# Performance work log

Measured on AMD Instinct MI355X. Metric: run time of the kernel, lower is better.

The kernel has to match this reference:

```python
import jax, jax.numpy as jnp
import numpy as np


def _conv(x, w):
    # stride-2, pad-1, 3x3 conv, NCHW activations, HWIO kernel
    return jax.lax.conv_general_dilated(
        x, w, (2, 2), [(1, 1), (1, 1)],
        dimension_numbers=('NCHW', 'HWIO', 'NCHW'))


def setup_inputs() -> dict:
    key = jax.random.key(0)
    ks = iter(jax.random.split(key, 40))
    def rn(shape, scale=1.0):
        return jax.random.normal(next(ks), shape, jnp.float32) * scale
    d = {}
    d['img'] = rn((64, 3, 128, 128))
    d['qst'] = rn((64, 128))
    d['conv_w0'] = rn((3, 3, 3, 24), 1.0 / np.sqrt(3 * 9))
    for i in (1, 2, 3):
        d['conv_w%d' % i] = rn((3, 3, 24, 24), 1.0 / np.sqrt(24 * 9))
    for i in range(4):
        d['bn_s%d' % i] = jax.random.uniform(next(ks), (24,), jnp.float32, 0.5, 1.5)
        d['bn_b%d' % i] = rn((24,), 0.1)
    d['g_w1'] = rn((180, 256), 1.0 / np.sqrt(180))
    d['g_b1'] = rn((256,), 0.01)
    for i in (2, 3, 4):
        d['g_w%d' % i] = rn((256, 256), 1.0 / np.sqrt(256))
        d['g_b%d' % i] = rn((256,), 0.01)
    d['f_w1'] = rn((256, 256), 1.0 / np.sqrt(256))
    d['f_b1'] = rn((256,), 0.01)
    d['f_w2'] = rn((256, 256), 1.0 / np.sqrt(256))
    d['f_b2'] = rn((256,), 0.01)
    d['cls_w'] = rn((256, 32), 1.0 / np.sqrt(256))
    d['cls_b'] = rn((32,), 0.01)
    return d


def reference(img, qst, conv_w0, conv_w1, conv_w2, conv_w3,
              bn_s0, bn_b0, bn_s1, bn_b1, bn_s2, bn_b2, bn_s3, bn_b3,
              g_w1, g_b1, g_w2, g_b2, g_w3, g_b3, g_w4, g_b4,
              f_w1, f_b1, f_w2, f_b2, cls_w, cls_b):
    x = img
    for w, s, b in ((conv_w0, bn_s0, bn_b0), (conv_w1, bn_s1, bn_b1),
                    (conv_w2, bn_s2, bn_b2), (conv_w3, bn_s3, bn_b3)):
        x = jax.nn.relu(_conv(x, w) * s[None, :, None, None] + b[None, :, None, None])
    N, C, H, W = x.shape  # [64, 24, 8, 8]
    # positional encoding: coords_x, coords_y in [-1,1]
    cx, cy = jnp.meshgrid(jnp.linspace(-1.0, 1.0, W), jnp.linspace(-1.0, 1.0, H))
    pos = jnp.broadcast_to(jnp.stack([cx, cy])[None], (N, 2, H, W)).astype(x.dtype)
    x = jnp.concatenate([x, pos], axis=1)              # [N, C+2, H, W]
    Cf = C + 2
    x = x.transpose(0, 2, 3, 1).reshape(N, H * W, Cf)  # [N, HW, 26]
    # RN_G first linear decomposed over concat([x_i, x_j, qst]) so the huge
    # [N, HW, HW, 2C+q] concat tensor is never materialized (same math).
    W1a, W1b, W1c = g_w1[:Cf], g_w1[Cf:2 * Cf], g_w1[2 * Cf:]
    hi = x @ W1a                      # [N, HW, 256]
    hj = x @ W1b                      # [N, HW, 256]
    hq = qst @ W1c + g_b1             # [N, 256]
    h = jax.nn.relu(hi[:, :, None, :] + hj[:, None, :, :] + hq[:, None, None, :])  # [N,HW,HW,256]
    h = jax.nn.relu(h @ g_w2 + g_b2)
    h = jax.nn.relu(h @ g_w3 + g_b3)
    h = jax.nn.relu(h @ g_w4 + g_b4)
    s = h.sum(axis=(1, 2))            # sum over all HW*HW pairs -> [N, 256]
    # RN_F (dropout is identity in eval mode)
    y = jax.nn.relu(s @ f_w1 + f_b1)
    y = jax.nn.relu(y @ f_w2 + f_b2)
    return jax.nn.log_softmax(y @ cls_w + cls_b, axis=1)
```

## Files before the change

### kernel.cpp

```cpp
#include <hip/hip_runtime.h>
#include <hip/hip_bf16.h>
#include <math.h>

typedef __bf16 bf16x8 __attribute__((ext_vector_type(8)));
typedef __bf16 bf16x4 __attribute__((ext_vector_type(4)));
typedef float  f32x4  __attribute__((ext_vector_type(4)));

#define LH 264

__global__ __launch_bounds__(256) void conv0_k(const float* __restrict__ x, const float* __restrict__ w,
                                               const float* __restrict__ sc, const float* __restrict__ bi,
                                               float* __restrict__ y) {
  const int H = 128, W = 128, OH = 64, OW = 64;
  __shared__ float wl[9 * 3 * 24];
  for (int i = threadIdx.x; i < 9 * 3 * 24; i += 256) wl[i] = w[i];
  __syncthreads();

  int idx = blockIdx.x * 256 + threadIdx.x;
  int oxh = idx & 31; int t = idx >> 5; int oy = t & 63; int n = t >> 6;
  int ox0 = oxh * 2;

  float acc0[24], acc1[24];
#pragma unroll
  for (int co = 0; co < 24; ++co) { acc0[co] = 0.f; acc1[co] = 0.f; }

  for (int ci = 0; ci < 3; ++ci) {
    const float* xp = x + (size_t)(n * 3 + ci) * H * W;
#pragma unroll
    for (int ky = 0; ky < 3; ++ky) {
      int iy = 2 * oy + ky - 1;
      if (iy < 0 || iy >= H) continue;
      const float* row = xp + (size_t)iy * W;
      int ixb = 2 * ox0 - 1;
      float in[7];
#pragma unroll
      for (int u = 0; u < 7; ++u) {
        int ix = ixb + u;
        in[u] = (ix >= 0 && ix < W) ? row[ix] : 0.f;
      }
#pragma unroll
      for (int kx = 0; kx < 3; ++kx) {
        const float* wp = &wl[((ky * 3 + kx) * 3 + ci) * 24];
        float v0 = in[kx], v1 = in[kx + 2];
#pragma unroll
        for (int co = 0; co < 24; ++co) {
          float wv = wp[co];
          acc0[co] += v0 * wv;
          acc1[co] += v1 * wv;
        }
      }
    }
  }
  float* yp = y + (size_t)n * 24 * OH * OW + (size_t)oy * OW + ox0;
#pragma unroll
  for (int co = 0; co < 24; ++co) {
    float s = sc[co], b = bi[co];
    yp[(size_t)co * OH * OW]     = fmaxf(acc0[co] * s + b, 0.f);
    yp[(size_t)co * OH * OW + 1] = fmaxf(acc1[co] * s + b, 0.f);
  }
}

__global__ __launch_bounds__(256) void conv1_k(const float* __restrict__ x, const float* __restrict__ w,
                                               const float* __restrict__ sc, const float* __restrict__ bi,
                                               float* __restrict__ y) {
  const int H = 64, W = 64, OH = 32, OW = 32;
  __shared__ float wl[9 * 24 * 12];
  const int half = blockIdx.x & 1, sb = blockIdx.x >> 1;
  for (int i = threadIdx.x; i < 2592; i += 256) {
    int co = i % 12, rest = i / 12;
    wl[i] = w[rest * 24 + half * 12 + co];
  }
  __syncthreads();

  int idx = sb * 256 + threadIdx.x;
  int oxh = idx & 15; int tt = idx >> 4; int oy = tt & 31; int n = tt >> 5;
  int ox0 = oxh * 2;

  float acc0[12], acc1[12];
#pragma unroll
  for (int co = 0; co < 12; ++co) { acc0[co] = 0.f; acc1[co] = 0.f; }

  for (int ci = 0; ci < 24; ++ci) {
    const float* xp = x + (size_t)(n * 24 + ci) * H * W;
#pragma unroll
    for (int ky = 0; ky < 3; ++ky) {
      int iy = 2 * oy + ky - 1;
      if (iy < 0 || iy >= H) continue;
      const float* row = xp + (size_t)iy * W;
      int ixb = 2 * ox0 - 1;
      float in[7];
#pragma unroll
      for (int u = 0; u < 7; ++u) {
        int ix = ixb + u;
        in[u] = (ix >= 0 && ix < W) ? row[ix] : 0.f;
      }
#pragma unroll
      for (int kx = 0; kx < 3; ++kx) {
        const float* wp = &wl[((ky * 3 + kx) * 24 + ci) * 12];
        float v0 = in[kx], v1 = in[kx + 2];
#pragma unroll
        for (int co = 0; co < 12; ++co) {
          float wv = wp[co];
          acc0[co] += v0 * wv;
          acc1[co] += v1 * wv;
        }
      }
    }
  }
  float* yp = y + (size_t)n * 24 * OH * OW + (size_t)(half * 12) * OH * OW + (size_t)oy * OW + ox0;
#pragma unroll
  for (int co = 0; co < 12; ++co) {
    int cog = half * 12 + co;
    float s = sc[cog], b = bi[cog];
    yp[(size_t)co * OH * OW]     = fmaxf(acc0[co] * s + b, 0.f);
    yp[(size_t)co * OH * OW + 1] = fmaxf(acc1[co] * s + b, 0.f);
  }
}

__global__ __launch_bounds__(256) void mid_k(const float* __restrict__ c1,
    const float* __restrict__ w2, const float* __restrict__ bs2, const float* __restrict__ bb2,
    const float* __restrict__ gw1, const float* __restrict__ gb1, const float* __restrict__ qst,
    const float* __restrict__ g2, const float* __restrict__ g3, const float* __restrict__ g4,
    float* __restrict__ c2, float* __restrict__ hq, __bf16* __restrict__ Wt,
    float* __restrict__ sbuf) {
  __shared__ float smem[8224];
  const int blk = blockIdx.x, t = threadIdx.x;

  if (blk < 128) {
    const int half = blk & 1, sb = blk >> 1;
    for (int i = t; i < 2592; i += 256) {
      int co = i % 12, rest = i / 12;
      smem[i] = w2[rest * 24 + half * 12 + co];
    }
    __syncthreads();
    int idx = sb * 256 + t;
    int ox = idx & 15, oy = (idx >> 4) & 15, n = idx >> 8;
    const int H = 32, W = 32, OH = 16, OW = 16;
    float acc[12];
#pragma unroll
    for (int co = 0; co < 12; ++co) acc[co] = 0.f;
    for (int ci = 0; ci < 24; ++ci) {
      const float* xp = c1 + (size_t)(n * 24 + ci) * H * W;
#pragma unroll
      for (int ky = 0; ky < 3; ++ky) {
        int iy = 2 * oy + ky - 1;
        if (iy < 0 || iy >= H) continue;
#pragma unroll
        for (int kx = 0; kx < 3; ++kx) {
          int ix = 2 * ox + kx - 1;
          if (ix < 0 || ix >= W) continue;
          float v = xp[(size_t)iy * W + ix];
          const float* wp = &smem[((ky * 3 + kx) * 24 + ci) * 12];
#pragma unroll
          for (int co = 0; co < 12; ++co) acc[co] += v * wp[co];
        }
      }
    }
    float* yp = c2 + (size_t)n * 24 * OH * OW + (size_t)(half * 12) * OH * OW + (size_t)oy * OW + ox;
#pragma unroll
    for (int co = 0; co < 12; ++co) {
      int cog = half * 12 + co;
      yp[(size_t)co * OH * OW] = fmaxf(acc[co] * bs2[cog] + bb2[cog], 0.f);
    }

  } else if (blk < 152) {
    float* tile = smem;
    const int lb = blk - 128;
    const int l = lb >> 3, ks = lb & 7;
    const float* src = (l == 0) ? g2 : (l == 1) ? g3 : g4;
    for (int kk = 0; kk < 32; ++kk) tile[kk * 257 + t] = src[(ks * 32 + kk) * 256 + t];
    __syncthreads();
    const int q = t & 3, nb = t >> 2;
    __bf16* out = Wt + (size_t)(l * 8 + ks) * 8192;
#pragma unroll
    for (int i = 0; i < 4; ++i) {
      int nn = i * 64 + nb;
      bf16x8 v;
#pragma unroll
      for (int j = 0; j < 8; ++j) v[j] = (__bf16)tile[(q * 8 + j) * 257 + nn];
      *(bf16x8*)&out[nn * 32 + q * 8] = v;
    }

  } else {
    const int n = blk - 152;
    sbuf[n * 256 + t] = 0.f;
    float* qs = smem;
    if (t < 128) qs[t] = qst[n * 128 + t];
    __syncthreads();
    float a = gb1[t];
    for (int c = 0; c < 128; ++c) a += qs[c] * gw1[(52 + c) * 256 + t];
    hq[n * 256 + t] = a;
  }
}

__global__ __launch_bounds__(256) void tail_k(const float* __restrict__ c2,
    const float* __restrict__ w3, const float* __restrict__ bs3, const float* __restrict__ bb3,
    const float* __restrict__ gw1, float* __restrict__ hi, float* __restrict__ hj) {
  __shared__ float w3l[5184];
  __shared__ float cs2[6144];
  __shared__ float s3[1536];
  const int n = blockIdx.x, t = threadIdx.x;
  for (int i = t; i < 5184; i += 256) w3l[i] = w3[i];
  for (int i = t; i < 6144; i += 256) cs2[i] = c2[(size_t)n * 6144 + i];
  __syncthreads();

  const int pos = t & 63, cog = t >> 6;
  const int oy = pos >> 3, ox = pos & 7;
  float acc[6];
#pragma unroll
  for (int u = 0; u < 6; ++u) acc[u] = 0.f;
  for (int ci = 0; ci < 24; ++ci) {
    const float* cp = &cs2[ci * 256];
#pragma unroll
    for (int ky = 0; ky < 3; ++ky) {
      int iy = 2 * oy + ky - 1;
      if (iy < 0 || iy >= 16) continue;
#pragma unroll
      for (int kx = 0; kx < 3; ++kx) {
        int ix = 2 * ox + kx - 1;
        if (ix < 0 || ix >= 16) continue;
        float v = cp[iy * 16 + ix];
        const float* wp = &w3l[((ky * 3 + kx) * 24 + ci) * 24 + cog * 6];
#pragma unroll
        for (int u = 0; u < 6; ++u) acc[u] += v * wp[u];
      }
    }
  }
#pragma unroll
  for (int u = 0; u < 6; ++u) {
    int co = cog * 6 + u;
    s3[co * 64 + pos] = fmaxf(acc[u] * bs3[co] + bb3[co], 0.f);
  }

  float wa[26], wb[26];
#pragma unroll
  for (int c = 0; c < 26; ++c) {
    wa[c] = gw1[c * 256 + t];
    wb[c] = gw1[(26 + c) * 256 + t];
  }
  __syncthreads();
  for (int p = 0; p < 64; ++p) {
    float a = 0.f, b = 0.f;
#pragma unroll
    for (int c = 0; c < 24; ++c) {
      float v = s3[c * 64 + p];
      a += v * wa[c];
      b += v * wb[c];
    }
    float cx = -1.f + (2.f / 7.f) * (float)(p & 7);
    float cy = -1.f + (2.f / 7.f) * (float)(p >> 3);
    a += cx * wa[24] + cy * wa[25];
    b += cx * wb[24] + cy * wb[25];
    hi[(size_t)(n * 64 + p) * 256 + t] = a;
    hj[(size_t)(n * 64 + p) * 256 + t] = b;
  }
}

__global__ __launch_bounds__(256, 2)
void g_fused(const float* __restrict__ hi, const float* __restrict__ hj,
             const float* __restrict__ hq, const __bf16* __restrict__ Wt,
             const float* __restrict__ b2, const float* __restrict__ b3,
             const float* __restrict__ b4, float* __restrict__ s_out) {
  const int blk = blockIdx.x;
  const int n = blk >> 5, ib = blk & 31;
  const int tid = threadIdx.x;
  const int wave = tid >> 6, lane = tid & 63;
  const int q = lane >> 4, lr = lane & 15;

  __shared__ __align__(16) __bf16 Hs[128 * LH];

  const int c0 = (tid & 63) * 4;
  float4 hq4 = *(const float4*)(hq + (size_t)n * 256 + c0);
  float4 h0 = *(const float4*)(hi + (size_t)(n * 64 + ib * 2)     * 256 + c0);
  float4 h1 = *(const float4*)(hi + (size_t)(n * 64 + ib * 2 + 1) * 256 + c0);
  h0.x += hq4.x; h0.y += hq4.y; h0.z += hq4.z; h0.w += hq4.w;
  h1.x += hq4.x; h1.y += hq4.y; h1.z += hq4.z; h1.w += hq4.w;

  const float* hjb = hj + (size_t)n * 64 * 256;
#pragma unroll
  for (int it = 0; it < 16; ++it) {
    int j = it * 4 + wave;
    float4 v = *(const float4*)(hjb + j * 256 + c0);
    bf16x4 o;
    o[0] = (__bf16)fmaxf(v.x + h0.x, 0.f);
    o[1] = (__bf16)fmaxf(v.y + h0.y, 0.f);
    o[2] = (__bf16)fmaxf(v.z + h0.z, 0.f);
    o[3] = (__bf16)fmaxf(v.w + h0.w, 0.f);
    *(bf16x4*)&Hs[j * LH + c0] = o;
    bf16x4 o2;
    o2[0] = (__bf16)fmaxf(v.x + h1.x, 0.f);
    o2[1] = (__bf16)fmaxf(v.y + h1.y, 0.f);
    o2[2] = (__bf16)fmaxf(v.z + h1.z, 0.f);
    o2[3] = (__bf16)fmaxf(v.w + h1.w, 0.f);
    *(bf16x4*)&Hs[(64 + j) * LH + c0] = o2;
  }
  __syncthreads();

  const int colloc = wave * 64 + lr;
  const __bf16* Bp = Wt + (size_t)wave * 2048 + lr * 32 + q * 8;

  for (int l = 0; l < 3; ++l) {
    const __bf16* Bl = Bp + (size_t)l * 65536;
    const float* bl = (l == 0) ? b2 : (l == 1) ? b3 : b4;

    f32x4 acc[8][4];
#pragma unroll
    for (int r = 0; r < 8; ++r)
#pragma unroll
      for (int c = 0; c < 4; ++c) acc[r][c] = (f32x4){0.f, 0.f, 0.f, 0.f};

    for (int ks = 0; ks < 8; ++ks) {
      bf16x8 b[4];
#pragma unroll
      for (int c = 0; c < 4; ++c)
        b[c] = *(const bf16x8*)&Bl[ks * 8192 + c * 512];
      bf16x8 a[8];
#pragma unroll
      for (int r = 0; r < 8; ++r)
        a[r] = *(const bf16x8*)&Hs[(r * 16 + lr) * LH + ks * 32 + q * 8];
#pragma unroll
      for (int r = 0; r < 8; ++r)
#pragma unroll
        for (int c = 0; c < 4; ++c)
          acc[r][c] = __builtin_amdgcn_mfma_f32_16x16x32_bf16(a[r], b[c], acc[r][c], 0, 0, 0);
    }

    float bias[4];
#pragma unroll
    for (int c = 0; c < 4; ++c) bias[c] = bl[colloc + c * 16];

    if (l < 2) {
      __syncthreads();
#pragma unroll
      for (int r = 0; r < 8; ++r)
#pragma unroll
        for (int c = 0; c < 4; ++c)
#pragma unroll
          for (int reg = 0; reg < 4; ++reg) {
            int row = r * 16 + q * 4 + reg;
            Hs[row * LH + colloc + c * 16] = (__bf16)fmaxf(acc[r][c][reg] + bias[c], 0.f);
          }
      __syncthreads();
    } else {
#pragma unroll
      for (int c = 0; c < 4; ++c) {
        float cs = 0.f;
#pragma unroll
        for (int r = 0; r < 8; ++r)
#pragma unroll
          for (int reg = 0; reg < 4; ++reg)
            cs += fmaxf(acc[r][c][reg] + bias[c], 0.f);
        cs += __shfl_xor(cs, 16);
        cs += __shfl_xor(cs, 32);
        if (q == 0) atomicAdd(&s_out[n * 256 + colloc + c * 16], cs);
      }
    }
  }
}

__global__ void f_net(const float* __restrict__ s, const float* __restrict__ fw1,
                      const float* __restrict__ fb1, const float* __restrict__ fw2,
                      const float* __restrict__ fb2, const float* __restrict__ cw,
                      const float* __restrict__ cb, float* __restrict__ out) {
  int n = blockIdx.x, t = threadIdx.x;
  __shared__ float buf[256], buf2[256], zs[32];
  buf[t] = s[n * 256 + t];
  __syncthreads();
  float a = fb1[t];
  for (int c = 0; c < 256; ++c) a += buf[c] * fw1[c * 256 + t];
  a = fmaxf(a, 0.f);
  buf2[t] = a;
  __syncthreads();
  float y = fb2[t];
  for (int c = 0; c < 256; ++c) y += buf2[c] * fw2[c * 256 + t];
  y = fmaxf(y, 0.f);
  __syncthreads();
  buf[t] = y;
  __syncthreads();
  float z = 0.f;
  if (t < 32) {
    z = cb[t];
    for (int c = 0; c < 256; ++c) z += buf[c] * cw[c * 32 + t];
    zs[t] = z;
  }
  __syncthreads();
  if (t < 32) {
    float m = -1e30f;
    for (int c = 0; c < 32; ++c) m = fmaxf(m, zs[c]);
    float se = 0.f;
    for (int c = 0; c < 32; ++c) se += expf(zs[c] - m);
    out[n * 32 + t] = z - m - logf(se);
  }
}

extern "C" void kernel_launch(void* const* d_in, const int* in_sizes, int n_in,
                              void* d_out, int out_size, void* d_ws, size_t ws_size,
                              hipStream_t stream) {
  const float* img  = (const float*)d_in[0];
  const float* qst  = (const float*)d_in[1];
  const float* w0   = (const float*)d_in[2];
  const float* w1   = (const float*)d_in[3];
  const float* w2   = (const float*)d_in[4];
  const float* w3   = (const float*)d_in[5];
  const float* bs0  = (const float*)d_in[6];
  const float* bb0  = (const float*)d_in[7];
  const float* bs1  = (const float*)d_in[8];
  const float* bb1  = (const float*)d_in[9];
  const float* bs2  = (const float*)d_in[10];
  const float* bb2  = (const float*)d_in[11];
  const float* bs3  = (const float*)d_in[12];
  const float* bb3  = (const float*)d_in[13];
  const float* gw1  = (const float*)d_in[14];
  const float* gb1  = (const float*)d_in[15];
  const float* gw2  = (const float*)d_in[16];
  const float* gb2  = (const float*)d_in[17];
  const float* gw3  = (const float*)d_in[18];
  const float* gb3  = (const float*)d_in[19];
  const float* gw4  = (const float*)d_in[20];
  const float* gb4  = (const float*)d_in[21];
  const float* fw1  = (const float*)d_in[22];
  const float* fb1  = (const float*)d_in[23];
  const float* fw2  = (const float*)d_in[24];
  const float* fb2  = (const float*)d_in[25];
  const float* cw   = (const float*)d_in[26];
  const float* cb   = (const float*)d_in[27];

  char* ws = (char*)d_ws;
  float* c0 = (float*)(ws + 0);
  float* c1 = (float*)(ws + 25165824);
  float* c2 = (float*)(ws + 31457280);
  float*  hi  = (float*)(ws + 0);
  float*  hj  = (float*)(ws + 4194304);
  float*  hqb = (float*)(ws + 8388608);
  float*  sbuf = (float*)(ws + 8454144);
  __bf16* Wt  = (__bf16*)(ws + 8519680);

  conv0_k<<<512, 256, 0, stream>>>(img, w0, bs0, bb0, c0);
  conv1_k<<<256, 256, 0, stream>>>(c0, w1, bs1, bb1, c1);
  mid_k<<<216, 256, 0, stream>>>(c1, w2, bs2, bb2, gw1, gb1, qst, gw2, gw3, gw4,
                                 c2, hqb, Wt, sbuf);
  tail_k<<<64, 256, 0, stream>>>(c2, w3, bs3, bb3, gw1, hi, hj);
  g_fused<<<2048, 256, 0, stream>>>(hi, hj, hqb, Wt, gb2, gb3, gb4, sbuf);
  f_net<<<64, 256, 0, stream>>>(sbuf, fw1, fb1, fw2, fb2, cw, cb, (float*)d_out);
}
```

Measured before the change: 316.7 us.

## Fuse conv2 into tail kernel, merge weight prep into conv0, retile g_fused waves

Moves the weight transpose, hq and sbuf-init work from mid_k into the conv0 launch as extra blocks. Fuses conv2 and conv3 into one per-image kernel that keeps the conv2 output in shared memory, which removes the c2 global round trip and one launch. Changes the g_fused wave tiling from 128x64 to 64x128 per wave, so each wave loads more B fragments and fewer A fragments. The risk is that the fused conv2 now runs on only 64 blocks with 24 accumulators per thread, where before it was spread across 128 blocks.

```diff
diff --git a/kernel.cpp b/kernel.cpp
--- a/kernel.cpp
+++ b/kernel.cpp
@@ -8,24 +8,111 @@
 
 #define LH 264
 
-__global__ __launch_bounds__(256) void conv0_k(const float* __restrict__ x, const float* __restrict__ w,
+__global__ __launch_bounds__(256) void k1(const float* __restrict__ img, const float* __restrict__ w0,
+    const float* __restrict__ bs0, const float* __restrict__ bb0,
+    const float* __restrict__ g2, const float* __restrict__ g3, const float* __restrict__ g4,
+    const float* __restrict__ gw1, const float* __restrict__ gb1, const float* __restrict__ qst,
+    float* __restrict__ c0, __bf16* __restrict__ Wt, float* __restrict__ hq,
+    float* __restrict__ sbuf) {
+  __shared__ __align__(16) float smem[8224];
+  const int blk = blockIdx.x, t = threadIdx.x;
+
+  if (blk < 512) {
+    float* wl = smem;
+    for (int i = t; i < 648; i += 256) wl[i] = w0[i];
+    __syncthreads();
+    const int H = 128, W = 128, OH = 64, OW = 64;
+    int idx = blk * 256 + t;
+    int oxh = idx & 31; int tt = idx >> 5; int oy = tt & 63; int n = tt >> 6;
+    int ox0 = oxh * 2;
+    float acc0[24], acc1[24];
+#pragma unroll
+    for (int co = 0; co < 24; ++co) { acc0[co] = 0.f; acc1[co] = 0.f; }
+    for (int ci = 0; ci < 3; ++ci) {
+      const float* xp = img + (size_t)(n * 3 + ci) * H * W;
+#pragma unroll
+      for (int ky = 0; ky < 3; ++ky) {
+        int iy = 2 * oy + ky - 1;
+        if (iy < 0 || iy >= H) continue;
+        const float* row = xp + (size_t)iy * W;
+        int ixb = 2 * ox0 - 1;
+        float in[7];
+#pragma unroll
+        for (int u = 0; u < 7; ++u) {
+          int ix = ixb + u;
+          in[u] = (ix >= 0 && ix < W) ? row[ix] : 0.f;
+        }
+#pragma unroll
+        for (int kx = 0; kx < 3; ++kx) {
+          const float* wp = &wl[((ky * 3 + kx) * 3 + ci) * 24];
+          float v0 = in[kx], v1 = in[kx + 2];
+#pragma unroll
+          for (int co = 0; co < 24; ++co) {
+            float wv = wp[co];
+            acc0[co] += v0 * wv;
+            acc1[co] += v1 * wv;
+          }
+        }
+      }
+    }
+    float* yp = c0 + (size_t)n * 24 * OH * OW + (size_t)oy * OW + ox0;
+#pragma unroll
+    for (int co = 0; co < 24; ++co) {
+      float s = bs0[co], b = bb0[co];
+      yp[(size_t)co * OH * OW]     = fmaxf(acc0[co] * s + b, 0.f);
+      yp[(size_t)co * OH * OW + 1] = fmaxf(acc1[co] * s + b, 0.f);
+    }
+  } else if (blk < 536) {
+    float* tile = smem;
+    const int lb = blk - 512;
+    const int l = lb >> 3, ks = lb & 7;
+    const float* src = (l == 0) ? g2 : (l == 1) ? g3 : g4;
+    for (int kk = 0; kk < 32; ++kk) tile[kk * 257 + t] = src[(ks * 32 + kk) * 256 + t];
+    __syncthreads();
+    const int q = t & 3, nb = t >> 2;
+    __bf16* out = Wt + (size_t)(l * 8 + ks) * 8192;
+#pragma unroll
+    for (int i = 0; i < 4; ++i) {
+      int nn = i * 64 + nb;
+      bf16x8 v;
+#pragma unroll
+      for (int j = 0; j < 8; ++j) v[j] = (__bf16)tile[(q * 8 + j) * 257 + nn];
+      *(bf16x8*)&out[nn * 32 + q * 8] = v;
+    }
+  } else {
+    float* qs = smem;
+    const int n = blk - 536;
+    sbuf[n * 256 + t] = 0.f;
+    if (t < 128) qs[t] = qst[n * 128 + t];
+    __syncthreads();
+    float a = gb1[t];
+    for (int c = 0; c < 128; ++c) a += qs[c] * gw1[(52 + c) * 256 + t];
+    hq[n * 256 + t] = a;
+  }
+}
+
+__global__ __launch_bounds__(256) void conv1_k(const float* __restrict__ x, const float* __restrict__ w,
                                                const float* __restrict__ sc, const float* __restrict__ bi,
                                                float* __restrict__ y) {
-  const int H = 128, W = 128, OH = 64, OW = 64;
-  __shared__ float wl[9 * 3 * 24];
-  for (int i = threadIdx.x; i < 9 * 3 * 24; i += 256) wl[i] = w[i];
-  __syncthreads();
-
-  int idx = blockIdx.x * 256 + threadIdx.x;
-  int oxh = idx & 31; int t = idx >> 5; int oy = t & 63; int n = t >> 6;
+  const int H = 64, W = 64, OH = 32, OW = 32;
+  __shared__ float wl[2592];
+  const int half = blockIdx.x & 1, sb = blockIdx.x >> 1;
+  for (int i = threadIdx.x; i < 2592; i += 256) {
+    int co = i % 12, rest = i / 12;
+    wl[i] = w[rest * 24 + half * 12 + co];
+  }
+  __syncthreads();
+
+  int idx = sb * 256 + threadIdx.x;
+  int oxh = idx & 15; int tt = idx >> 4; int oy = tt & 31; int n = tt >> 5;
   int ox0 = oxh * 2;
 
-  float acc0[24], acc1[24];
-#pragma unroll
-  for (int co = 0; co < 24; ++co) { acc0[co] = 0.f; acc1[co] = 0.f; }
-
-  for (int ci = 0; ci < 3; ++ci) {
-    const float* xp = x + (size_t)(n * 3 + ci) * H * W;
+  float acc0[12], acc1[12];
+#pragma unroll
+  for (int co = 0; co < 12; ++co) { acc0[co] = 0.f; acc1[co] = 0.f; }
+
+  for (int ci = 0; ci < 24; ++ci) {
+    const float* xp = x + (size_t)(n * 24 + ci) * H * W;
 #pragma unroll
     for (int ky = 0; ky < 3; ++ky) {
       int iy = 2 * oy + ky - 1;
@@ -40,62 +127,6 @@
       }
 #pragma unroll
       for (int kx = 0; kx < 3; ++kx) {
-        const float* wp = &wl[((ky * 3 + kx) * 3 + ci) * 24];
-        float v0 = in[kx], v1 = in[kx + 2];
-#pragma unroll
-        for (int co = 0; co < 24; ++co) {
-          float wv = wp[co];
-          acc0[co] += v0 * wv;
-          acc1[co] += v1 * wv;
-        }
-      }
-    }
-  }
-  float* yp = y + (size_t)n * 24 * OH * OW + (size_t)oy * OW + ox0;
-#pragma unroll
-  for (int co = 0; co < 24; ++co) {
-    float s = sc[co], b = bi[co];
-    yp[(size_t)co * OH * OW]     = fmaxf(acc0[co] * s + b, 0.f);
-    yp[(size_t)co * OH * OW + 1] = fmaxf(acc1[co] * s + b, 0.f);
-  }
-}
-
-__global__ __launch_bounds__(256) void conv1_k(const float* __restrict__ x, const float* __restrict__ w,
-                                               const float* __restrict__ sc, const float* __restrict__ bi,
-                                               float* __restrict__ y) {
-  const int H = 64, W = 64, OH = 32, OW = 32;
-  __shared__ float wl[9 * 24 * 12];
-  const int half = blockIdx.x & 1, sb = blockIdx.x >> 1;
-  for (int i = threadIdx.x; i < 2592; i += 256) {
-    int co = i % 12, rest = i / 12;
-    wl[i] = w[rest * 24 + half * 12 + co];
-  }
-  __syncthreads();
-
-  int idx = sb * 256 + threadIdx.x;
-  int oxh = idx & 15; int tt = idx >> 4; int oy = tt & 31; int n = tt >> 5;
-  int ox0 = oxh * 2;
-
-  float acc0[12], acc1[12];
-#pragma unroll
-  for (int co = 0; co < 12; ++co) { acc0[co] = 0.f; acc1[co] = 0.f; }
-
-  for (int ci = 0; ci < 24; ++ci) {
-    const float* xp = x + (size_t)(n * 24 + ci) * H * W;
-#pragma unroll
-    for (int ky = 0; ky < 3; ++ky) {
-      int iy = 2 * oy + ky - 1;
-      if (iy < 0 || iy >= H) continue;
-      const float* row = xp + (size_t)iy * W;
-      int ixb = 2 * ox0 - 1;
-      float in[7];
-#pragma unroll
-      for (int u = 0; u < 7; ++u) {
-        int ix = ixb + u;
-        in[u] = (ix >= 0 && ix < W) ? row[ix] : 0.f;
-      }
-#pragma unroll
-      for (int kx = 0; kx < 3; ++kx) {
         const float* wp = &wl[((ky * 3 + kx) * 24 + ci) * 12];
         float v0 = in[kx], v1 = in[kx + 2];
 #pragma unroll
@@ -117,121 +148,74 @@
   }
 }
 
-__global__ __launch_bounds__(256) void mid_k(const float* __restrict__ c1,
+__global__ __launch_bounds__(256) void chain2_k(const float* __restrict__ c1,
     const float* __restrict__ w2, const float* __restrict__ bs2, const float* __restrict__ bb2,
-    const float* __restrict__ gw1, const float* __restrict__ gb1, const float* __restrict__ qst,
-    const float* __restrict__ g2, const float* __restrict__ g3, const float* __restrict__ g4,
-    float* __restrict__ c2, float* __restrict__ hq, __bf16* __restrict__ Wt,
-    float* __restrict__ sbuf) {
-  __shared__ float smem[8224];
-  const int blk = blockIdx.x, t = threadIdx.x;
-
-  if (blk < 128) {
-    const int half = blk & 1, sb = blk >> 1;
-    for (int i = t; i < 2592; i += 256) {
-      int co = i % 12, rest = i / 12;
-      smem[i] = w2[rest * 24 + half * 12 + co];
-    }
-    __syncthreads();
-    int idx = sb * 256 + t;
-    int ox = idx & 15, oy = (idx >> 4) & 15, n = idx >> 8;
-    const int H = 32, W = 32, OH = 16, OW = 16;
-    float acc[12];
-#pragma unroll
-    for (int co = 0; co < 12; ++co) acc[co] = 0.f;
+    const float* __restrict__ w3, const float* __restrict__ bs3, const float* __restrict__ bb3,
+    const float* __restrict__ gw1, float* __restrict__ hi, float* __restrict__ hj) {
+  __shared__ float sw[5184];
+  __shared__ float s2[6144];
+  __shared__ float s3[1536];
+  const int n = blockIdx.x, t = threadIdx.x;
+  for (int i = t; i < 5184; i += 256) sw[i] = w2[i];
+  __syncthreads();
+  {
+    int ox = t & 15, oy = t >> 4;
+    float acc[24];
+#pragma unroll
+    for (int co = 0; co < 24; ++co) acc[co] = 0.f;
     for (int ci = 0; ci < 24; ++ci) {
-      const float* xp = c1 + (size_t)(n * 24 + ci) * H * W;
+      const float* xp = c1 + (size_t)(n * 24 + ci) * 1024;
 #pragma unroll
       for (int ky = 0; ky < 3; ++ky) {
         int iy = 2 * oy + ky - 1;
-        if (iy < 0 || iy >= H) continue;
+        if (iy < 0 || iy >= 32) continue;
 #pragma unroll
         for (int kx = 0; kx < 3; ++kx) {
           int ix = 2 * ox + kx - 1;
-          if (ix < 0 || ix >= W) continue;
-          float v = xp[(size_t)iy * W + ix];
-          const float* wp = &smem[((ky * 3 + kx) * 24 + ci) * 12];
-#pragma unroll
-          for (int co = 0; co < 12; ++co) acc[co] += v * wp[co];
+          if (ix < 0 || ix >= 32) continue;
+          float v = xp[iy * 32 + ix];
+          const float* wp = &sw[((ky * 3 + kx) * 24 + ci) * 24];
+#pragma unroll
+          for (int co = 0; co < 24; ++co) acc[co] += v * wp[co];
         }
       }
     }
-    float* yp = c2 + (size_t)n * 24 * OH * OW + (size_t)(half * 12) * OH * OW + (size_t)oy * OW + ox;
-#pragma unroll
-    for (int co = 0; co < 12; ++co) {
-      int cog = half * 12 + co;
-      yp[(size_t)co * OH * OW] = fmaxf(acc[co] * bs2[cog] + bb2[cog], 0.f);
-    }
-
-  } else if (blk < 152) {
-    float* tile = smem;
-    const int lb = blk - 128;
-    const int l = lb >> 3, ks = lb & 7;
-    const float* src = (l == 0) ? g2 : (l == 1) ? g3 : g4;
-    for (int kk = 0; kk < 32; ++kk) tile[kk * 257 + t] = src[(ks * 32 + kk) * 256 + t];
-    __syncthreads();
-    const int q = t & 3, nb = t >> 2;
-    __bf16* out = Wt + (size_t)(l * 8 + ks) * 8192;
-#pragma unroll
-    for (int i = 0; i < 4; ++i) {
-      int nn = i * 64 + nb;
-      bf16x8 v;
-#pragma unroll
-      for (int j = 0; j < 8; ++j) v[j] = (__bf16)tile[(q * 8 + j) * 257 + nn];
-      *(bf16x8*)&out[nn * 32 + q * 8] = v;
-    }
-
-  } else {
-    const int n = blk - 152;
-    sbuf[n * 256 + t] = 0.f;
-    float* qs = smem;
-    if (t < 128) qs[t] = qst[n * 128 + t];
-    __syncthreads();
-    float a = gb1[t];
-    for (int c = 0; c < 128; ++c) a += qs[c] * gw1[(52 + c) * 256 + t];
-    hq[n * 256 + t] = a;
-  }
-}
-
-__global__ __launch_bounds__(256) void tail_k(const float* __restrict__ c2,
-    const float* __restrict__ w3, const float* __restrict__ bs3, const float* __restrict__ bb3,
-    const float* __restrict__ gw1, float* __restrict__ hi, float* __restrict__ hj) {
-  __shared__ float w3l[5184];
-  __shared__ float cs2[6144];
-  __shared__ float s3[1536];
-  const int n = blockIdx.x, t = threadIdx.x;
-  for (int i = t; i < 5184; i += 256) w3l[i] = w3[i];
-  for (int i = t; i < 6144; i += 256) cs2[i] = c2[(size_t)n * 6144 + i];
-  __syncthreads();
-
-  const int pos = t & 63, cog = t >> 6;
-  const int oy = pos >> 3, ox = pos & 7;
-  float acc[6];
-#pragma unroll
-  for (int u = 0; u < 6; ++u) acc[u] = 0.f;
-  for (int ci = 0; ci < 24; ++ci) {
-    const float* cp = &cs2[ci * 256];
-#pragma unroll
-    for (int ky = 0; ky < 3; ++ky) {
-      int iy = 2 * oy + ky - 1;
-      if (iy < 0 || iy >= 16) continue;
-#pragma unroll
-      for (int kx = 0; kx < 3; ++kx) {
-        int ix = 2 * ox + kx - 1;
-        if (ix < 0 || ix >= 16) continue;
-        float v = cp[iy * 16 + ix];
-        const float* wp = &w3l[((ky * 3 + kx) * 24 + ci) * 24 + cog * 6];
-#pragma unroll
-        for (int u = 0; u < 6; ++u) acc[u] += v * wp[u];
-      }
-    }
-  }
-#pragma unroll
-  for (int u = 0; u < 6; ++u) {
-    int co = cog * 6 + u;
-    s3[co * 64 + pos] = fmaxf(acc[u] * bs3[co] + bb3[co], 0.f);
-  }
-
+#pragma unroll
+    for (int co = 0; co < 24; ++co)
+      s2[co * 256 + t] = fmaxf(acc[co] * bs2[co] + bb2[co], 0.f);
+  }
+  __syncthreads();
+  for (int i = t; i < 5184; i += 256) sw[i] = w3[i];
+  __syncthreads();
+  {
+    const int pos = t & 63, cog = t >> 6;
+    const int oy = pos >> 3, ox = pos & 7;
+    float acc[6];
+#pragma unroll
+    for (int u = 0; u < 6; ++u) acc[u] = 0.f;
+    for (int ci = 0; ci < 24; ++ci) {
+      const float* cp = &s2[ci * 256];
+#pragma unroll
+      for (int ky = 0; ky < 3; ++ky) {
+        int iy = 2 * oy + ky - 1;
+        if (iy < 0 || iy >= 16) continue;
+#pragma unroll
+        for (int kx = 0; kx < 3; ++kx) {
+          int ix = 2 * ox + kx - 1;
+          if (ix < 0 || ix >= 16) continue;
+          float v = cp[iy * 16 + ix];
+          const float* wp = &sw[((ky * 3 + kx) * 24 + ci) * 24 + cog * 6];
+#pragma unroll
+          for (int u = 0; u < 6; ++u) acc[u] += v * wp[u];
+        }
+      }
+    }
+#pragma unroll
+    for (int u = 0; u < 6; ++u) {
+      int co = cog * 6 + u;
+      s3[co * 64 + pos] = fmaxf(acc[u] * bs3[co] + bb3[co], 0.f);
+    }
+  }
   float wa[26], wb[26];
 #pragma unroll
   for (int c = 0; c < 26; ++c) {
@@ -296,63 +280,64 @@
   }
   __syncthreads();
 
-  const int colloc = wave * 64 + lr;
-  const __bf16* Bp = Wt + (size_t)wave * 2048 + lr * 32 + q * 8;
+  const int rbase = (wave >> 1) * 64;
+  const int cbase = (wave & 1) * 128;
+  const __bf16* Bp = Wt + (size_t)cbase * 32 + lr * 32 + q * 8;
 
   for (int l = 0; l < 3; ++l) {
     const __bf16* Bl = Bp + (size_t)l * 65536;
     const float* bl = (l == 0) ? b2 : (l == 1) ? b3 : b4;
 
-    f32x4 acc[8][4];
-#pragma unroll
-    for (int r = 0; r < 8; ++r)
-#pragma unroll
-      for (int c = 0; c < 4; ++c) acc[r][c] = (f32x4){0.f, 0.f, 0.f, 0.f};
+    f32x4 acc[4][8];
+#pragma unroll
+    for (int r = 0; r < 4; ++r)
+#pragma unroll
+      for (int c = 0; c < 8; ++c) acc[r][c] = (f32x4){0.f, 0.f, 0.f, 0.f};
 
     for (int ks = 0; ks < 8; ++ks) {
-      bf16x8 b[4];
-#pragma unroll
-      for (int c = 0; c < 4; ++c)
+      bf16x8 b[8];
+#pragma unroll
+      for (int c = 0; c < 8; ++c)
         b[c] = *(const bf16x8*)&Bl[ks * 8192 + c * 512];
-      bf16x8 a[8];
-#pragma unroll
-      for (int r = 0; r < 8; ++r)
-        a[r] = *(const bf16x8*)&Hs[(r * 16 + lr) * LH + ks * 32 + q * 8];
-#pragma unroll
-      for (int r = 0; r < 8; ++r)
-#pragma unroll
-        for (int c = 0; c < 4; ++c)
+      bf16x8 a[4];
+#pragma unroll
+      for (int r = 0; r < 4; ++r)
+        a[r] = *(const bf16x8*)&Hs[(rbase + r * 16 + lr) * LH + ks * 32 + q * 8];
+#pragma unroll
+      for (int r = 0; r < 4; ++r)
+#pragma unroll
+        for (int c = 0; c < 8; ++c)
           acc[r][c] = __builtin_amdgcn_mfma_f32_16x16x32_bf16(a[r], b[c], acc[r][c], 0, 0, 0);
     }
 
-    float bias[4];
-#pragma unroll
-    for (int c = 0; c < 4; ++c) bias[c] = bl[colloc + c * 16];
+    float bias[8];
+#pragma unroll
+    for (int c = 0; c < 8; ++c) bias[c] = bl[cbase + c * 16 + lr];
 
     if (l < 2) {
       __syncthreads();
 #pragma unroll
-      for (int r = 0; r < 8; ++r)
-#pragma unroll
-        for (int c = 0; c < 4; ++c)
+      for (int r = 0; r < 4; ++r)
+#pragma unroll
+        for (int c = 0; c < 8; ++c)
 #pragma unroll
           for (int reg = 0; reg < 4; ++reg) {
-            int row = r * 16 + q * 4 + reg;
-            Hs[row * LH + colloc + c * 16] = (__bf16)fmaxf(acc[r][c][reg] + bias[c], 0.f);
+            int row = rbase + r * 16 + q * 4 + reg;
+            Hs[row * LH + cbase + c * 16 + lr] = (__bf16)fmaxf(acc[r][c][reg] + bias[c], 0.f);
           }
       __syncthreads();
     } else {
 #pragma unroll
-      for (int c = 0; c < 4; ++c) {
+      for (int c = 0; c < 8; ++c) {
         float cs = 0.f;
 #pragma unroll
-        for (int r = 0; r < 8; ++r)
+        for (int r = 0; r < 4; ++r)
 #pragma unroll
           for (int reg = 0; reg < 4; ++reg)
             cs += fmaxf(acc[r][c][reg] + bias[c], 0.f);
         cs += __shfl_xor(cs, 16);
         cs += __shfl_xor(cs, 32);
-        if (q == 0) atomicAdd(&s_out[n * 256 + colloc + c * 16], cs);
+        if (q == 0) atomicAdd(&s_out[n * 256 + cbase + c * 16 + lr], cs);
       }
     }
   }
@@ -428,18 +413,16 @@
   char* ws = (char*)d_ws;
   float* c0 = (float*)(ws + 0);
   float* c1 = (float*)(ws + 25165824);
-  float* c2 = (float*)(ws + 31457280);
+  __bf16* Wt  = (__bf16*)(ws + 31457280);
+  float*  hqb = (float*)(ws + 31850496);
+  float*  sbuf = (float*)(ws + 31916032);
   float*  hi  = (float*)(ws + 0);
   float*  hj  = (float*)(ws + 4194304);
-  float*  hqb = (float*)(ws + 8388608);
-  float*  sbuf = (float*)(ws + 8454144);
-  __bf16* Wt  = (__bf16*)(ws + 8519680);
-
-  conv0_k<<<512, 256, 0, stream>>>(img, w0, bs0, bb0, c0);
+
+  k1<<<600, 256, 0, stream>>>(img, w0, bs0, bb0, gw2, gw3, gw4, gw1, gb1, qst,
+                              c0, Wt, hqb, sbuf);
   conv1_k<<<256, 256, 0, stream>>>(c0, w1, bs1, bb1, c1);
-  mid_k<<<216, 256, 0, stream>>>(c1, w2, bs2, bb2, gw1, gb1, qst, gw2, gw3, gw4,
-                                 c2, hqb, Wt, sbuf);
-  tail_k<<<64, 256, 0, stream>>>(c2, w3, bs3, bb3, gw1, hi, hj);
+  chain2_k<<<64, 256, 0, stream>>>(c1, w2, bs2, bb2, w3, bs3, bb3, gw1, hi, hj);
   g_fused<<<2048, 256, 0, stream>>>(hi, hj, hqb, Wt, gb2, gb3, gb4, sbuf);
   f_net<<<64, 256, 0, stream>>>(sbuf, fw1, fb1, fw2, fb2, cw, cb, (float*)d_out);
 }
```

Result: slower. 361.5 us (+14.2%).
